# Optimization experiments

Hardware: AMD Instinct MI355X
Metric: run time of the kernel (lower is better)

## Reference

```python
import jax, jax.numpy as jnp
import numpy as np

N_NODES = 50000
N_EDGES = 1600000
D = 128
LEAKY_SLOPE = 0.01  # torch nn.LeakyReLU default


def setup_inputs() -> dict:
    key = jax.random.key(0)
    ks = jax.random.split(key, 7)
    entity_embed = jax.random.normal(ks[0], (N_NODES, D), dtype=jnp.float32)
    W1 = jax.random.normal(ks[1], (D, D), dtype=jnp.float32) * 0.05
    b1 = jax.random.normal(ks[2], (D,), dtype=jnp.float32) * 0.05
    W2 = jax.random.normal(ks[3], (D, D), dtype=jnp.float32) * 0.05
    b2 = jax.random.normal(ks[4], (D,), dtype=jnp.float32) * 0.05
    src = jax.random.randint(ks[5], (N_EDGES,), 0, N_NODES, dtype=jnp.int32)
    dst = jax.random.randint(ks[6], (N_EDGES,), 0, N_NODES, dtype=jnp.int32)
    return {"entity_embed": entity_embed, "W1": W1, "b1": b1,
            "W2": W2, "b2": b2, "src": src, "dst": dst}


def reference(entity_embed, W1, b1, W2, b2, src, dst):
    # DGL update_all(copy_u('node','side'), sum('side','H')):
    # H[v] = sum over edges (u -> v) of entity_embed[u]
    n = entity_embed.shape[0]
    H = jax.ops.segment_sum(entity_embed[src], dst, num_segments=n)  # [N, D]
    # neighbors branch: LeakyReLU(W_1 @ H)
    neighbors = jax.nn.leaky_relu(H @ W1.T + b1, negative_slope=LEAKY_SLOPE)
    # interactions branch: LeakyReLU(W_2 @ (node * H))
    interactions = jax.nn.leaky_relu((entity_embed * H) @ W2.T + b2,
                                     negative_slope=LEAKY_SLOPE)
    # dropout is identity at inference
    return neighbors + interactions
```

## Files before the change

### kernel.cpp

```cpp
#include <hip/hip_runtime.h>

#define NN 50000
#define DD 128
#define SLOPE 0.01f
#define NB 782
#define BCAP 2304
#define NSB 49
#define SBW 1024
#define SCAP 34816
#define ECH1 4096
#define RSL 2048
#define RS 17
#define OVCAP 8192
#define HP 136

using bf16x8 = __attribute__((ext_vector_type(8))) short;
using f32x4  = __attribute__((ext_vector_type(4))) float;

__device__ inline float bflo(unsigned int w) { return __uint_as_float(w << 16); }
__device__ inline float bfhi(unsigned int w) { return __uint_as_float(w & 0xffff0000u); }
__device__ inline float sbf(short s) {
    return __uint_as_float(((unsigned int)(unsigned short)s) << 16);
}
__device__ inline unsigned int rnebf(float f) {
    unsigned int u = __float_as_uint(f);
    return (u + 0x7fffu + ((u >> 16) & 1u)) >> 16;
}
__device__ inline unsigned int pack2(float lo, float hi) {
    return rnebf(lo) | (rnebf(hi) << 16);
}
__device__ inline void addrow(float* acc, uint4 r) {
    acc[0] += bflo(r.x); acc[1] += bfhi(r.x);
    acc[2] += bflo(r.y); acc[3] += bfhi(r.y);
    acc[4] += bflo(r.z); acc[5] += bfhi(r.z);
    acc[6] += bflo(r.w); acc[7] += bfhi(r.w);
}

__device__ inline void convert_item(
    const float* __restrict__ E, const float* __restrict__ W1,
    const float* __restrict__ W2, unsigned short* __restrict__ Ebf,
    unsigned short* __restrict__ W1b, unsigned short* __restrict__ W2b, int t)
{
    const int NE8 = NN * DD / 8;
    const int NW8 = DD * DD / 8;
    const float* s; unsigned short* d; int idx;
    if (t < NE8)                { s = E;  d = Ebf; idx = t; }
    else if (t < NE8 + NW8)     { s = W1; d = W1b; idx = t - NE8; }
    else if (t < NE8 + 2 * NW8) { s = W2; d = W2b; idx = t - NE8 - NW8; }
    else return;
    float4 a = ((const float4*)s)[(size_t)idx * 2];
    float4 b = ((const float4*)s)[(size_t)idx * 2 + 1];
    uint4 o;
    o.x = pack2(a.x, a.y); o.y = pack2(a.z, a.w);
    o.z = pack2(b.x, b.y); o.w = pack2(b.z, b.w);
    ((uint4*)d)[idx] = o;
}

__global__ __launch_bounds__(512) void scatter_convert(
    const float* __restrict__ E, const float* __restrict__ W1,
    const float* __restrict__ W2, const int* __restrict__ src,
    const int* __restrict__ dst, unsigned short* __restrict__ Ebf,
    unsigned short* __restrict__ W1b, unsigned short* __restrict__ W2b,
    int* __restrict__ gtail1, unsigned int* __restrict__ stag1,
    int* __restrict__ ovf_cnt, int2* __restrict__ ovf,
    int n_edges, int nch1)
{
    const int tid = threadIdx.x;
    if (blockIdx.x >= nch1) {
        convert_item(E, W1, W2, Ebf, W1b, W2b,
                     (blockIdx.x - nch1) * 512 + tid);
        return;
    }

    __shared__ int cnt49[NSB];
    const int e0 = blockIdx.x * ECH1;
    int vv[8], uu[8];

    if (tid < NSB) cnt49[tid] = 0;
    __syncthreads();
    #pragma unroll
    for (int k = 0; k < 8; ++k) {
        int idx = e0 + tid + k * 512;
        if (idx < n_edges) {
            vv[k] = dst[idx]; uu[k] = src[idx];
            atomicAdd(&cnt49[vv[k] >> 10], 1);
        } else vv[k] = -1;
    }
    __syncthreads();
    if (tid < NSB) {
        int c = cnt49[tid];
        cnt49[tid] = c ? atomicAdd(&gtail1[tid], c) : 0;
    }
    __syncthreads();
    #pragma unroll
    for (int k = 0; k < 8; ++k) {
        if (vv[k] < 0) continue;
        int sb = vv[k] >> 10;
        int p = atomicAdd(&cnt49[sb], 1);
        if (p < SCAP) {
            stag1[(size_t)sb * SCAP + p] =
                (unsigned int)uu[k] | ((unsigned int)(vv[k] & 1023) << 16);
        } else {
            int oi = atomicAdd(ovf_cnt, 1);
            if (oi < OVCAP) ovf[oi] = make_int2(uu[k], vv[k]);
        }
    }
}

__global__ __launch_bounds__(256) void rebin(
    const int* __restrict__ gtail1, const unsigned int* __restrict__ stag1,
    int* __restrict__ gtail, unsigned int* __restrict__ stag,
    int* __restrict__ ovf_cnt, int2* __restrict__ ovf)
{
    const int sb = blockIdx.x / RS, sl = blockIdx.x % RS;
    const int tid = threadIdx.x;
    int len = gtail1[sb]; len = len < SCAP ? len : SCAP;
    const int i0 = sl * RSL;
    const int i1 = min(i0 + RSL, len);

    __shared__ int cnt16[16], pos16[16];
    if (tid < 16) cnt16[tid] = 0;
    __syncthreads();

    unsigned int r[8];
    const unsigned int* seg = stag1 + (size_t)sb * SCAP;
    #pragma unroll
    for (int k = 0; k < 8; ++k) {
        int idx = i0 + tid + k * 256;
        if (idx < i1) {
            r[k] = seg[idx];
            atomicAdd(&cnt16[(r[k] >> 22) & 15], 1);
        } else r[k] = 0xffffffffu;
    }
    __syncthreads();
    if (tid < 16) {
        int c = cnt16[tid];
        int bb = sb * 16 + tid;
        pos16[tid] = (c && bb < NB) ? atomicAdd(&gtail[bb], c) : 0;
    }
    __syncthreads();
    #pragma unroll
    for (int k = 0; k < 8; ++k) {
        if (r[k] == 0xffffffffu) continue;
        int j = (r[k] >> 22) & 15;
        int p = atomicAdd(&pos16[j], 1);
        int bb = sb * 16 + j;
        if (p < BCAP) {
            stag[(size_t)bb * BCAP + p] = r[k] & 0x3fffffu;
        } else {
            int oi = atomicAdd(ovf_cnt, 1);
            if (oi < OVCAP)
                ovf[oi] = make_int2((int)(r[k] & 0xffffu),
                                    sb * SBW + (int)((r[k] >> 16) & 1023));
        }
    }
}

__global__ __launch_bounds__(256, 4) void bucket_gather(
    const unsigned short* __restrict__ Ebf, const int* __restrict__ gtail,
    const unsigned int* __restrict__ stag, const int* __restrict__ ovf_cnt,
    const int2* __restrict__ ovf, float* __restrict__ Hf)
{
    __shared__ unsigned short sorted[BCAP];
    __shared__ int cnt1k[1024];
    __shared__ int bstart[1025];
    __shared__ int wsum[4];
    __shared__ int s_novf;

    const int b = blockIdx.x >> 1;
    const int h = blockIdx.x & 1;
    const int tid = threadIdx.x;
    int len = gtail[b]; len = len < BCAP ? len : BCAP;
    const unsigned int* seg = stag + (size_t)b * BCAP;

    if (tid == 0) { int t = *ovf_cnt; s_novf = t < OVCAP ? t : OVCAP; }
    #pragma unroll
    for (int j = 0; j < 4; ++j) cnt1k[tid * 4 + j] = 0;
    __syncthreads();
    for (int i = tid; i < len; i += 256) {
        unsigned int r = seg[i];
        int key = (int)(((r >> 16) & 63) << 4) | (int)((r & 0xffffu) >> 12);
        atomicAdd(&cnt1k[key], 1);
    }
    __syncthreads();
    {
        const int lane = tid & 63, w = tid >> 6;
        int c[4], loc[4]; int s = 0;
        #pragma unroll
        for (int j = 0; j < 4; ++j) {
            c[j] = cnt1k[tid * 4 + j]; loc[j] = s; s += c[j];
        }
        int incl = s;
        #pragma unroll
        for (int d = 1; d < 64; d <<= 1) {
            int t2 = __shfl_up(incl, d);
            if (lane >= d) incl += t2;
        }
        if (lane == 63) wsum[w] = incl;
        __syncthreads();
        int wbase = 0;
        for (int w2 = 0; w2 < w; ++w2) wbase += wsum[w2];
        int base = wbase + incl - s;
        #pragma unroll
        for (int j = 0; j < 4; ++j) {
            bstart[tid * 4 + j] = base + loc[j];
            cnt1k[tid * 4 + j]  = base + loc[j];
        }
        if (tid == 255) bstart[1024] = base + s;
    }
    __syncthreads();
    for (int i = tid; i < len; i += 256) {
        unsigned int r = seg[i];
        int key = (int)(((r >> 16) & 63) << 4) | (int)((r & 0xffffu) >> 12);
        int p = atomicAdd(&cnt1k[key], 1);
        sorted[p] = (unsigned short)(r & 0xffffu);
    }
    __syncthreads();
    const int novf = s_novf;

    const int g = tid >> 3;
    const int c = tid & 7;
    const uint4* E4 = (const uint4*)Ebf;
    for (int p2 = 0; p2 < 2; ++p2) {
        int nl = p2 * 32 + g;
        int v = b * 64 + nl;
        if (v >= NN) continue;
        float acc[8] = {};
        int i = bstart[nl << 4], e1 = bstart[(nl + 1) << 4];
        uint4 r[8];
        for (; i + 8 <= e1; i += 8) {
            #pragma unroll
            for (int k = 0; k < 8; ++k)
                r[k] = E4[(size_t)sorted[i + k] * 16 + h * 8 + c];
            __builtin_amdgcn_sched_barrier(0);
            #pragma unroll
            for (int k = 0; k < 8; ++k) addrow(acc, r[k]);
        }
        for (; i + 2 <= e1; i += 2) {
            uint4 r0 = E4[(size_t)sorted[i]     * 16 + h * 8 + c];
            uint4 r1 = E4[(size_t)sorted[i + 1] * 16 + h * 8 + c];
            addrow(acc, r0); addrow(acc, r1);
        }
        if (i < e1) addrow(acc, E4[(size_t)sorted[i] * 16 + h * 8 + c]);

        if (novf > 0) {
            for (int k = 0; k < novf; ++k) {
                int2 e = ovf[k];
                if (e.y == v) addrow(acc, E4[(size_t)e.x * 16 + h * 8 + c]);
            }
        }
        float* o = Hf + (size_t)v * DD + h * 64 + c * 8;
        *(float4*)o       = make_float4(acc[0], acc[1], acc[2], acc[3]);
        *(float4*)(o + 4) = make_float4(acc[4], acc[5], acc[6], acc[7]);
    }
}

__global__ __launch_bounds__(256) void bucket_gemm(
    const float* __restrict__ Hf, const unsigned short* __restrict__ Ebf,
    const unsigned short* __restrict__ W1b, const unsigned short* __restrict__ W2b,
    const float* __restrict__ b1, const float* __restrict__ b2,
    float* __restrict__ out)
{
    const int b = blockIdx.x;
    const int tid = threadIdx.x;
    const int wave = tid >> 6;
    const int lane = tid & 63;
    const int v0 = b * 64 + wave * 16;
    if (v0 >= NN) return;
    const int m = lane & 15;
    const int quad = lane >> 4;

    bf16x8 aH[4], aE[4];
    const float* hrow = Hf + (size_t)(v0 + m) * DD + quad * 8;
    const unsigned short* erow = Ebf + (size_t)(v0 + m) * DD + quad * 8;
    #pragma unroll
    for (int ks = 0; ks < 4; ++ks) {
        float4 f0 = *(const float4*)(hrow + ks * 32);
        float4 f1 = *(const float4*)(hrow + ks * 32 + 4);
        bf16x8 e8 = *(const bf16x8*)(erow + ks * 32);
        bf16x8 h8, eh;
        h8[0] = (short)rnebf(f0.x); h8[1] = (short)rnebf(f0.y);
        h8[2] = (short)rnebf(f0.z); h8[3] = (short)rnebf(f0.w);
        h8[4] = (short)rnebf(f1.x); h8[5] = (short)rnebf(f1.y);
        h8[6] = (short)rnebf(f1.z); h8[7] = (short)rnebf(f1.w);
        #pragma unroll
        for (int j = 0; j < 8; ++j)
            eh[j] = (short)rnebf(sbf(h8[j]) * sbf(e8[j]));
        aH[ks] = h8; aE[ks] = eh;
    }

    #pragma unroll
    for (int jt = 0; jt < 8; ++jt) {
        const int j0 = jt * 16;
        const unsigned short* w1r = W1b + (size_t)(j0 + m) * DD + quad * 8;
        const unsigned short* w2r = W2b + (size_t)(j0 + m) * DD + quad * 8;
        f32x4 acc1 = {0.f, 0.f, 0.f, 0.f}, acc2 = {0.f, 0.f, 0.f, 0.f};
        #pragma unroll
        for (int ks = 0; ks < 4; ++ks) {
            bf16x8 bw1 = *(const bf16x8*)(w1r + ks * 32);
            bf16x8 bw2 = *(const bf16x8*)(w2r + ks * 32);
            acc1 = __builtin_amdgcn_mfma_f32_16x16x32_bf16(aH[ks], bw1, acc1, 0, 0, 0);
            acc2 = __builtin_amdgcn_mfma_f32_16x16x32_bf16(aE[ks], bw2, acc2, 0, 0, 0);
        }
        const float bb1 = b1[j0 + m], bb2 = b2[j0 + m];
        #pragma unroll
        for (int i = 0; i < 4; ++i) {
            int row = v0 + quad * 4 + i;
            if (row < NN) {
                float x1 = acc1[i] + bb1; x1 = x1 > 0.f ? x1 : SLOPE * x1;
                float x2 = acc2[i] + bb2; x2 = x2 > 0.f ? x2 : SLOPE * x2;
                out[(size_t)row * DD + j0 + m] = x1 + x2;
            }
        }
    }
}

__global__ __launch_bounds__(256, 4) void bucket_fused(
    const unsigned short* __restrict__ Ebf, const int* __restrict__ gtail,
    const unsigned int* __restrict__ stag, const int* __restrict__ ovf_cnt,
    const int2* __restrict__ ovf,
    const unsigned short* __restrict__ W1b, const unsigned short* __restrict__ W2b,
    const float* __restrict__ b1, const float* __restrict__ b2,
    float* __restrict__ out)
{
    __shared__ unsigned short sorted[BCAP];
    __shared__ unsigned short Hs[64][HP];
    __shared__ int cnt[64], off[65], pos[64];
    __shared__ int s_novf;

    const int b = blockIdx.x;
    const int tid = threadIdx.x;
    int len = gtail[b]; len = len < BCAP ? len : BCAP;
    const unsigned int* seg = stag + (size_t)b * BCAP;

    if (tid == 0) { int t = *ovf_cnt; s_novf = t < OVCAP ? t : OVCAP; }
    if (tid < 64) cnt[tid] = 0;
    __syncthreads();
    for (int i = tid; i < len; i += 256)
        atomicAdd(&cnt[(seg[i] >> 16) & 63], 1);
    __syncthreads();
    if (tid < 64) {
        int cv = cnt[tid];
        int incl = cv;
        #pragma unroll
        for (int d = 1; d < 64; d <<= 1) {
            int t2 = __shfl_up(incl, d);
            if (tid >= d) incl += t2;
        }
        off[tid] = incl - cv;
        pos[tid] = incl - cv;
        if (tid == 63) off[64] = incl;
    }
    __syncthreads();
    for (int i = tid; i < len; i += 256) {
        unsigned int r = seg[i];
        int p = atomicAdd(&pos[(r >> 16) & 63], 1);
        sorted[p] = (unsigned short)(r & 0xffffu);
    }
    __syncthreads();
    const int novf = s_novf;

    const int g = tid >> 4;
    const int c = tid & 15;
    const uint4* E4 = (const uint4*)Ebf;
    for (int p4 = 0; p4 < 4; ++p4) {
        int nl = p4 * 16 + g;
        int v = b * 64 + nl;
        if (v >= NN) continue;
        float acc[8] = {};
        int i = off[nl], e1 = off[nl + 1];
        uint4 r[8];
        for (; i + 8 <= e1; i += 8) {
            #pragma unroll
            for (int k = 0; k < 8; ++k)
                r[k] = E4[(size_t)sorted[i + k] * 16 + c];
            __builtin_amdgcn_sched_barrier(0);
            #pragma unroll
            for (int k = 0; k < 8; ++k) addrow(acc, r[k]);
        }
        for (; i + 2 <= e1; i += 2) {
            uint4 r0 = E4[(size_t)sorted[i]     * 16 + c];
            uint4 r1 = E4[(size_t)sorted[i + 1] * 16 + c];
            addrow(acc, r0); addrow(acc, r1);
        }
        if (i < e1) addrow(acc, E4[(size_t)sorted[i] * 16 + c]);
        if (novf > 0) {
            for (int k = 0; k < novf; ++k) {
                int2 e = ovf[k];
                if (e.y == v) addrow(acc, E4[(size_t)e.x * 16 + c]);
            }
        }
        uint4 o;
        o.x = pack2(acc[0], acc[1]); o.y = pack2(acc[2], acc[3]);
        o.z = pack2(acc[4], acc[5]); o.w = pack2(acc[6], acc[7]);
        *(uint4*)&Hs[nl][c * 8] = o;
    }
    __syncthreads();

    const int wave = tid >> 6;
    const int lane = tid & 63;
    const int v0 = b * 64 + wave * 16;
    if (v0 >= NN) return;
    const int m = lane & 15;
    const int quad = lane >> 4;

    bf16x8 aH[4], aE[4];
    const unsigned short* hrow = &Hs[wave * 16 + m][quad * 8];
    const unsigned short* erow = Ebf + (size_t)(v0 + m) * DD + quad * 8;
    #pragma unroll
    for (int ks = 0; ks < 4; ++ks) {
        bf16x8 h8 = *(const bf16x8*)(hrow + ks * 32);
        bf16x8 e8 = *(const bf16x8*)(erow + ks * 32);
        aH[ks] = h8;
        bf16x8 eh;
        #pragma unroll
        for (int j = 0; j < 8; ++j)
            eh[j] = (short)rnebf(sbf(h8[j]) * sbf(e8[j]));
        aE[ks] = eh;
    }
    #pragma unroll
    for (int jt = 0; jt < 8; ++jt) {
        const int j0 = jt * 16;
        const unsigned short* w1r = W1b + (size_t)(j0 + m) * DD + quad * 8;
        const unsigned short* w2r = W2b + (size_t)(j0 + m) * DD + quad * 8;
        f32x4 acc1 = {0.f, 0.f, 0.f, 0.f}, acc2 = {0.f, 0.f, 0.f, 0.f};
        #pragma unroll
        for (int ks = 0; ks < 4; ++ks) {
            bf16x8 bw1 = *(const bf16x8*)(w1r + ks * 32);
            bf16x8 bw2 = *(const bf16x8*)(w2r + ks * 32);
            acc1 = __builtin_amdgcn_mfma_f32_16x16x32_bf16(aH[ks], bw1, acc1, 0, 0, 0);
            acc2 = __builtin_amdgcn_mfma_f32_16x16x32_bf16(aE[ks], bw2, acc2, 0, 0, 0);
        }
        const float bb1 = b1[j0 + m], bb2 = b2[j0 + m];
        #pragma unroll
        for (int i = 0; i < 4; ++i) {
            int row = v0 + quad * 4 + i;
            if (row < NN) {
                float x1 = acc1[i] + bb1; x1 = x1 > 0.f ? x1 : SLOPE * x1;
                float x2 = acc2[i] + bb2; x2 = x2 > 0.f ? x2 : SLOPE * x2;
                out[(size_t)row * DD + j0 + m] = x1 + x2;
            }
        }
    }
}

__global__ __launch_bounds__(256) void scatter_add(
    const float* __restrict__ E, const int* __restrict__ src,
    const int* __restrict__ dst, float* __restrict__ H, int n_edges)
{
    int t = blockIdx.x * 256 + threadIdx.x;
    int e = t >> 5;
    if (e >= n_edges) return;
    int c = t & 31;
    float4 a = ((const float4*)E)[(size_t)src[e] * 32 + c];
    float* hp = H + (size_t)dst[e] * DD + c * 4;
    atomicAdd(hp + 0, a.x); atomicAdd(hp + 1, a.y);
    atomicAdd(hp + 2, a.z); atomicAdd(hp + 3, a.w);
}

__global__ __launch_bounds__(256) void fused_mlp(
    const float* __restrict__ E, const float* __restrict__ H,
    const float* __restrict__ W1, const float* __restrict__ b1,
    const float* __restrict__ W2, const float* __restrict__ b2,
    float* __restrict__ out)
{
    __shared__ float Hsf[32][DD];
    __shared__ float EHs[32][DD];
    __shared__ float W1s[DD][20];
    __shared__ float W2s[DD][20];
    const int tid = threadIdx.x;
    const int v0 = blockIdx.x * 32;
    const int nvalid = min(32, NN - v0);
    for (int i = 0; i < 4; ++i) {
        int f = tid + 256 * i;
        int n = f >> 5, c = f & 31;
        float4 h = make_float4(0.f, 0.f, 0.f, 0.f);
        float4 eh = h;
        if (n < nvalid) {
            h = ((const float4*)H)[(size_t)(v0 + n) * 32 + c];
            float4 e4 = ((const float4*)E)[(size_t)(v0 + n) * 32 + c];
            eh = make_float4(e4.x * h.x, e4.y * h.y, e4.z * h.z, e4.w * h.w);
        }
        *((float4*)&Hsf[n][c * 4]) = h;
        *((float4*)&EHs[n][c * 4]) = eh;
    }
    const int jg = tid & 63;
    const int n0 = (tid >> 6) * 8;
    float acc1a[8] = {}, acc1b[8] = {}, acc2a[8] = {}, acc2b[8] = {};
    for (int t8 = 0; t8 < 8; ++t8) {
        const int k0 = t8 * 16;
        __syncthreads();
        for (int i = 0; i < 8; ++i) {
            int f = tid + 256 * i;
            int j = f >> 4, kk = f & 15;
            W1s[j][kk] = W1[j * DD + k0 + kk];
            W2s[j][kk] = W2[j * DD + k0 + kk];
        }
        __syncthreads();
        for (int c = 0; c < 4; ++c) {
            float4 w1a = *((const float4*)&W1s[jg][c * 4]);
            float4 w1b = *((const float4*)&W1s[jg + 64][c * 4]);
            float4 w2a = *((const float4*)&W2s[jg][c * 4]);
            float4 w2b = *((const float4*)&W2s[jg + 64][c * 4]);
            const int kk = k0 + c * 4;
            for (int n = 0; n < 8; ++n) {
                float4 h = *((const float4*)&Hsf[n0 + n][kk]);
                float4 eh = *((const float4*)&EHs[n0 + n][kk]);
                acc1a[n] += h.x * w1a.x + h.y * w1a.y + h.z * w1a.z + h.w * w1a.w;
                acc1b[n] += h.x * w1b.x + h.y * w1b.y + h.z * w1b.z + h.w * w1b.w;
                acc2a[n] += eh.x * w2a.x + eh.y * w2a.y + eh.z * w2a.z + eh.w * w2a.w;
                acc2b[n] += eh.x * w2b.x + eh.y * w2b.y + eh.z * w2b.z + eh.w * w2b.w;
            }
        }
    }
    const float b1a = b1[jg], b1b = b1[jg + 64];
    const float b2a = b2[jg], b2b = b2[jg + 64];
    for (int n = 0; n < 8; ++n) {
        if (n0 + n < nvalid) {
            const int v = v0 + n0 + n;
            float x1 = acc1a[n] + b1a; x1 = x1 > 0.f ? x1 : SLOPE * x1;
            float x2 = acc2a[n] + b2a; x2 = x2 > 0.f ? x2 : SLOPE * x2;
            out[(size_t)v * DD + jg] = x1 + x2;
            float y1 = acc1b[n] + b1b; y1 = y1 > 0.f ? y1 : SLOPE * y1;
            float y2 = acc2b[n] + b2b; y2 = y2 > 0.f ? y2 : SLOPE * y2;
            out[(size_t)v * DD + jg + 64] = y1 + y2;
        }
    }
}

extern "C" void kernel_launch(void* const* d_in, const int* in_sizes, int n_in,
                              void* d_out, int out_size, void* d_ws, size_t ws_size,
                              hipStream_t stream)
{
    const float* E  = (const float*)d_in[0];
    const float* W1 = (const float*)d_in[1];
    const float* b1 = (const float*)d_in[2];
    const float* W2 = (const float*)d_in[3];
    const float* b2 = (const float*)d_in[4];
    const int* src  = (const int*)d_in[5];
    const int* dst  = (const int*)d_in[6];
    float* out = (float*)d_out;
    const int n_edges = in_sizes[5];

    char* ws = (char*)d_ws;
    auto al = [](size_t x) { return (x + 255) & ~(size_t)255; };

    const int nch1 = (n_edges + ECH1 - 1) / ECH1;

    const size_t ctr_ints  = NSB + 1 + NB;
    const size_t off_ovf   = al(ctr_ints * 4);
    const size_t off_stag1 = al(off_ovf + (size_t)OVCAP * 8);
    const size_t off_stag  = al(off_stag1 + (size_t)NSB * SCAP * 4);
    const size_t off_Ebf   = al(off_stag + (size_t)NB * BCAP * 4);
    const size_t off_W1b   = al(off_Ebf + (size_t)NN * DD * 2);
    const size_t off_W2b   = al(off_W1b + (size_t)DD * DD * 2);
    const size_t need_bf   = off_W2b + (size_t)DD * DD * 2;
    const size_t off_Hf    = al(need_bf);
    const size_t need_split = off_Hf + (size_t)NN * DD * 4;

    if (ws_size >= need_bf) {
        int*  gtail1  = (int*)ws;
        int*  ovf_cnt = gtail1 + NSB;
        int*  gtail   = gtail1 + NSB + 1;
        int2* ovf     = (int2*)(ws + off_ovf);
        unsigned int*   stag1 = (unsigned int*)(ws + off_stag1);
        unsigned int*   stag  = (unsigned int*)(ws + off_stag);
        unsigned short* Ebf   = (unsigned short*)(ws + off_Ebf);
        unsigned short* W1b   = (unsigned short*)(ws + off_W1b);
        unsigned short* W2b   = (unsigned short*)(ws + off_W2b);

        const int NCV  = NN * DD / 8 + 2 * (DD * DD / 8);
        const int ncvb = (NCV + 511) / 512;

        hipMemsetAsync(ws, 0, ctr_ints * 4, stream);
        scatter_convert<<<nch1 + ncvb, 512, 0, stream>>>(
            E, W1, W2, src, dst, Ebf, W1b, W2b,
            gtail1, stag1, ovf_cnt, ovf, n_edges, nch1);
        rebin<<<NSB * RS, 256, 0, stream>>>(
            gtail1, stag1, gtail, stag, ovf_cnt, ovf);

        if (ws_size >= need_split) {
            float* Hf = (float*)(ws + off_Hf);
            bucket_gather<<<NB * 2, 256, 0, stream>>>(
                Ebf, gtail, stag, ovf_cnt, ovf, Hf);
            bucket_gemm<<<NB, 256, 0, stream>>>(
                Hf, Ebf, W1b, W2b, b1, b2, out);
        } else {
            bucket_fused<<<NB, 256, 0, stream>>>(
                Ebf, gtail, stag, ovf_cnt, ovf, W1b, W2b, b1, b2, out);
        }
        return;
    }

    const size_t hbytes = (size_t)NN * DD * sizeof(float);
    float* H = (ws_size >= hbytes) ? (float*)ws : out;
    hipMemsetAsync(H, 0, hbytes, stream);
    scatter_add<<<((n_edges * 32) + 255) / 256, 256, 0, stream>>>(
        E, src, dst, H, n_edges);
    fused_mlp<<<(NN + 31) / 32, 256, 0, stream>>>(E, H, W1, b1, W2, b2, out);
}
```

Measured before the change: 193.5 us.

## Split gather by source-row range across XCD-mapped blocks with partial H buffers

```diff
diff --git a/kernel.cpp b/kernel.cpp
--- a/kernel.cpp
+++ b/kernel.cpp
@@ -13,6 +13,7 @@
 #define RS 17
 #define OVCAP 8192
 #define HP 136
+#define SROW0 24576
 
 using bf16x8 = __attribute__((ext_vector_type(8))) short;
 using f32x4  = __attribute__((ext_vector_type(4))) float;
@@ -159,7 +160,7 @@
 __global__ __launch_bounds__(256, 4) void bucket_gather(
     const unsigned short* __restrict__ Ebf, const int* __restrict__ gtail,
     const unsigned int* __restrict__ stag, const int* __restrict__ ovf_cnt,
-    const int2* __restrict__ ovf, float* __restrict__ Hf)
+    const int2* __restrict__ ovf, float* __restrict__ Hf, int npart)
 {
     __shared__ unsigned short sorted[BCAP];
     __shared__ int cnt1k[1024];
@@ -167,8 +168,17 @@
     __shared__ int wsum[4];
     __shared__ int s_novf;
 
-    const int b = blockIdx.x >> 1;
-    const int h = blockIdx.x & 1;
+    int b, h, s;
+    if (npart == 2) {
+        const int xcd  = blockIdx.x & 7;
+        const int slot = blockIdx.x >> 3;
+        const int q    = xcd >> 1;
+        h = q & 1; s = q >> 1;
+        b = slot * 2 + (xcd & 1);
+        if (b >= NB) return;
+    } else {
+        b = blockIdx.x >> 1; h = blockIdx.x & 1; s = 0;
+    }
     const int tid = threadIdx.x;
     int len = gtail[b]; len = len < BCAP ? len : BCAP;
     const unsigned int* seg = stag + (size_t)b * BCAP;
@@ -185,12 +195,12 @@
     __syncthreads();
     {
         const int lane = tid & 63, w = tid >> 6;
-        int c[4], loc[4]; int s = 0;
+        int c[4], loc[4]; int ss = 0;
         #pragma unroll
         for (int j = 0; j < 4; ++j) {
-            c[j] = cnt1k[tid * 4 + j]; loc[j] = s; s += c[j];
-        }
-        int incl = s;
+            c[j] = cnt1k[tid * 4 + j]; loc[j] = ss; ss += c[j];
+        }
+        int incl = ss;
         #pragma unroll
         for (int d = 1; d < 64; d <<= 1) {
             int t2 = __shfl_up(incl, d);
@@ -200,13 +210,13 @@
         __syncthreads();
         int wbase = 0;
         for (int w2 = 0; w2 < w; ++w2) wbase += wsum[w2];
-        int base = wbase + incl - s;
+        int base = wbase + incl - ss;
         #pragma unroll
         for (int j = 0; j < 4; ++j) {
             bstart[tid * 4 + j] = base + loc[j];
             cnt1k[tid * 4 + j]  = base + loc[j];
         }
-        if (tid == 255) bstart[1024] = base + s;
+        if (tid == 255) bstart[1024] = base + ss;
     }
     __syncthreads();
     for (int i = tid; i < len; i += 256) {
@@ -217,6 +227,8 @@
     }
     __syncthreads();
     const int novf = s_novf;
+
+    float* Hq = Hf + (size_t)s * NN * DD;
 
     const int g = tid >> 3;
     const int c = tid & 7;
@@ -226,7 +238,9 @@
         int v = b * 64 + nl;
         if (v >= NN) continue;
         float acc[8] = {};
-        int i = bstart[nl << 4], e1 = bstart[(nl + 1) << 4];
+        int lo = nl * 16, hi = nl * 16 + 16;
+        if (npart == 2) { if (s == 0) hi = nl * 16 + 6; else lo = nl * 16 + 6; }
+        int i = bstart[lo], e1 = bstart[hi];
         uint4 r[8];
         for (; i + 8 <= e1; i += 8) {
             #pragma unroll
@@ -246,10 +260,12 @@
         if (novf > 0) {
             for (int k = 0; k < novf; ++k) {
                 int2 e = ovf[k];
-                if (e.y == v) addrow(acc, E4[(size_t)e.x * 16 + h * 8 + c]);
+                if (e.y != v) continue;
+                if (npart == 2 && ((e.x >= SROW0) ? 1 : 0) != s) continue;
+                addrow(acc, E4[(size_t)e.x * 16 + h * 8 + c]);
             }
         }
-        float* o = Hf + (size_t)v * DD + h * 64 + c * 8;
+        float* o = Hq + (size_t)v * DD + h * 64 + c * 8;
         *(float4*)o       = make_float4(acc[0], acc[1], acc[2], acc[3]);
         *(float4*)(o + 4) = make_float4(acc[4], acc[5], acc[6], acc[7]);
     }
@@ -259,7 +275,7 @@
     const float* __restrict__ Hf, const unsigned short* __restrict__ Ebf,
     const unsigned short* __restrict__ W1b, const unsigned short* __restrict__ W2b,
     const float* __restrict__ b1, const float* __restrict__ b2,
-    float* __restrict__ out)
+    float* __restrict__ out, int npart)
 {
     const int b = blockIdx.x;
     const int tid = threadIdx.x;
@@ -271,12 +287,19 @@
     const int quad = lane >> 4;
 
     bf16x8 aH[4], aE[4];
-    const float* hrow = Hf + (size_t)(v0 + m) * DD + quad * 8;
+    const float* hrow  = Hf + (size_t)(v0 + m) * DD + quad * 8;
+    const float* hrow2 = hrow + (size_t)NN * DD;
     const unsigned short* erow = Ebf + (size_t)(v0 + m) * DD + quad * 8;
     #pragma unroll
     for (int ks = 0; ks < 4; ++ks) {
         float4 f0 = *(const float4*)(hrow + ks * 32);
         float4 f1 = *(const float4*)(hrow + ks * 32 + 4);
+        if (npart == 2) {
+            float4 g0 = *(const float4*)(hrow2 + ks * 32);
+            float4 g1 = *(const float4*)(hrow2 + ks * 32 + 4);
+            f0.x += g0.x; f0.y += g0.y; f0.z += g0.z; f0.w += g0.w;
+            f1.x += g1.x; f1.y += g1.y; f1.z += g1.z; f1.w += g1.w;
+        }
         bf16x8 e8 = *(const bf16x8*)(erow + ks * 32);
         bf16x8 h8, eh;
         h8[0] = (short)rnebf(f0.x); h8[1] = (short)rnebf(f0.y);
@@ -556,7 +579,8 @@
     const size_t off_W2b   = al(off_W1b + (size_t)DD * DD * 2);
     const size_t need_bf   = off_W2b + (size_t)DD * DD * 2;
     const size_t off_Hf    = al(need_bf);
-    const size_t need_split = off_Hf + (size_t)NN * DD * 4;
+    const size_t need_sp1  = off_Hf + (size_t)NN * DD * 4;
+    const size_t need_sp2  = off_Hf + (size_t)NN * DD * 8;
 
     if (ws_size >= need_bf) {
         int*  gtail1  = (int*)ws;
@@ -579,12 +603,14 @@
         rebin<<<NSB * RS, 256, 0, stream>>>(
             gtail1, stag1, gtail, stag, ovf_cnt, ovf);
 
-        if (ws_size >= need_split) {
+        if (ws_size >= need_sp1) {
             float* Hf = (float*)(ws + off_Hf);
-            bucket_gather<<<NB * 2, 256, 0, stream>>>(
-                Ebf, gtail, stag, ovf_cnt, ovf, Hf);
+            const int npart = (ws_size >= need_sp2) ? 2 : 1;
+            const int ggrid = (npart == 2) ? 8 * 392 : NB * 2;
+            bucket_gather<<<ggrid, 256, 0, stream>>>(
+                Ebf, gtail, stag, ovf_cnt, ovf, Hf, npart);
             bucket_gemm<<<NB, 256, 0, stream>>>(
-                Hf, Ebf, W1b, W2b, b1, b2, out);
+                Hf, Ebf, W1b, W2b, b1, b2, out, npart);
         } else {
             bucket_fused<<<NB, 256, 0, stream>>>(
                 Ebf, gtail, stag, ovf_cnt, ovf, W1b, W2b, b1, b2, out);
```

Result: slower. 203.2 us (+5.0%).
